# Kernel optimization log

Hardware: AMD Instinct MI355X
Metric: run time of the kernel (lower is better)

The kernel has to match this reference:

```python
import jax, jax.numpy as jnp
import numpy as np

N_NODES = 100000

def gcn_conv(x, edge_index, W, b, n_nodes):
    # GCNConv: add self-loops, symmetric normalization D^-1/2 A D^-1/2, then linear.
    loops = jnp.arange(n_nodes, dtype=edge_index.dtype)
    row = jnp.concatenate([edge_index[0], loops])  # source nodes
    col = jnp.concatenate([edge_index[1], loops])  # destination nodes
    deg = jax.ops.segment_sum(jnp.ones_like(col, dtype=x.dtype), col, num_segments=n_nodes)
    dinv = jnp.where(deg > 0, jax.lax.rsqrt(deg), 0.0)
    norm = dinv[row] * dinv[col]                   # [E']
    h = x @ W                                      # [N, out] project first (out dim small)
    msgs = h[row] * norm[:, None]                  # gather + scale
    out = jax.ops.segment_sum(msgs, col, num_segments=n_nodes)  # scatter-add
    return out + b

def setup_inputs() -> dict:
    key = jax.random.key(0)
    k1, k2, k3, k4, k5, k6 = jax.random.split(key, 6)
    in_dim, hid, out_dim = 512, 16, 16
    x = jax.random.normal(k1, (N_NODES, in_dim), dtype=jnp.float32)
    edge_index = jax.random.randint(k2, (2, 3200000), 0, N_NODES, dtype=jnp.int64)
    # Glorot-style init for weights, zero bias (GCNConv defaults)
    W1 = jax.random.normal(k3, (in_dim, hid), dtype=jnp.float32) * (1.0 / np.sqrt(in_dim))
    b1 = jnp.zeros((hid,), dtype=jnp.float32)
    W2 = jax.random.normal(k4, (hid, out_dim), dtype=jnp.float32) * (1.0 / np.sqrt(hid))
    b2 = jnp.zeros((out_dim,), dtype=jnp.float32)
    return {"x": x, "edge_index": edge_index, "W1": W1, "b1": b1, "W2": W2, "b2": b2}

def reference(x, edge_index, W1, b1, W2, b2):
    h = jax.nn.relu(gcn_conv(x, edge_index, W1, b1, N_NODES))
    # dropout is identity in eval mode
    logits = gcn_conv(h, edge_index, W2, b2, N_NODES)
    return jax.nn.log_softmax(logits, axis=1)
```

## Files before the change

### kernel.cpp

```cpp
#include <hip/hip_runtime.h>
#include <cstddef>

typedef unsigned int uint32;
typedef short bf16x8 __attribute__((ext_vector_type(8)));
typedef float f32x4 __attribute__((ext_vector_type(4)));

#define BCAP 5120

__device__ __forceinline__ unsigned short f2bf(float f) {
  unsigned u = __float_as_uint(f);
  unsigned r = (u + 0x7FFFu + ((u >> 16) & 1u)) >> 16;
  return (unsigned short)r;
}
__device__ __forceinline__ float bf_lo(uint32 u) { return __uint_as_float(u << 16); }
__device__ __forceinline__ float bf_hi(uint32 u) { return __uint_as_float(u & 0xFFFF0000u); }

__global__ __launch_bounds__(256) void k_init(
    int* __restrict__ bcur, int NB, const float* __restrict__ W1,
    unsigned short* __restrict__ wfrag) {
  int zb = (NB + 255) >> 8;
  int b = blockIdx.x;
  if (b < zb) {
    int i = b * 256 + threadIdx.x;
    if (i < NB) bcur[i] = i * BCAP;
  } else {
    int i = (b - zb) * 256 + threadIdx.x;
    if (i < 8192) {
      int j = i & 7, o = (i >> 3) & 15, g = (i >> 7) & 3, kt = i >> 9;
      wfrag[i] = f2bf(W1[(kt * 32 + g * 8 + j) * 16 + o]);
    }
  }
}

__global__ __launch_bounds__(256) void k_bfill(
    const int* __restrict__ row, const int* __restrict__ col,
    int* __restrict__ bcur, int* __restrict__ bedges, int E, int NB, int chunk) {
  __shared__ int s[1024];
  for (int j = threadIdx.x; j < NB; j += 256) s[j] = 0;
  __syncthreads();
  int lo = blockIdx.x * chunk;
  int hi = lo + chunk; if (hi > E) hi = E;
  for (int k = lo + threadIdx.x; k < hi; k += 256) atomicAdd(&s[col[k] >> 7], 1);
  __syncthreads();
  for (int j = threadIdx.x; j < NB; j += 256) {
    int h = s[j];
    s[j] = h ? atomicAdd(&bcur[j], h) : 0;
  }
  __syncthreads();
  for (int k = lo + threadIdx.x; k < hi; k += 256) {
    int c = col[k];
    int b = c >> 7;
    int slot = atomicAdd(&s[b], 1);
    if (slot < (b + 1) * BCAP)
      bedges[slot] = ((c & 127) << 17) | row[k];
  }
}

__global__ __launch_bounds__(128) void k_bdeg(
    const int* __restrict__ bcur, const int* __restrict__ bedges,
    float* __restrict__ dinv, int n) {
  __shared__ int c[128];
  int b = blockIdx.x, t = threadIdx.x;
  c[t] = 0;
  __syncthreads();
  int k0 = b * BCAP;
  int k1 = bcur[b]; if (k1 > k0 + BCAP) k1 = k0 + BCAP;
  for (int k = k0 + t; k < k1; k += 128)
    atomicAdd(&c[((unsigned)bedges[k]) >> 17], 1);
  __syncthreads();
  int node = b * 128 + t;
  if (node < n) dinv[node] = rsqrtf(1.0f + (float)c[t]);
}

#define GCAP 2048
#define CAPL 48
template <int MODE>
__global__ __launch_bounds__(256) void k_gagg(
    const int* __restrict__ bcur, const int* __restrict__ bedges,
    const uint4* __restrict__ mb,
    float* __restrict__ agg, unsigned short* __restrict__ msgs_out,
    const float* __restrict__ dinv, const float* __restrict__ b1,
    const float* __restrict__ W2, const float* __restrict__ b2, int n) {
  __shared__ int lsrt[CAPL * 128];
  __shared__ int curs[128];
  __shared__ int ovf[128];
  __shared__ int novf;
  __shared__ float w2s[256];
  __shared__ float b1s[16];
  int b = blockIdx.x, t = threadIdx.x;
  if (MODE == 1) {
    w2s[t] = W2[t];
    if (t < 16) b1s[t] = b1[t];
  }
  int j = t >> 1, h = t & 1;
  int node = b * 128 + j;
  float a0 = 0.f, a1 = 0.f, a2 = 0.f, a3 = 0.f;
  float a4 = 0.f, a5 = 0.f, a6 = 0.f, a7 = 0.f;
  if (node < n) {
    float4 sA = *(const float4*)(agg + (size_t)node * 16 + h * 8);
    float4 sB = *(const float4*)(agg + (size_t)node * 16 + h * 8 + 4);
    a0 = sA.x; a1 = sA.y; a2 = sA.z; a3 = sA.w;
    a4 = sB.x; a5 = sB.y; a6 = sB.z; a7 = sB.w;
  }
  int k0 = b * BCAP;
  int k1 = bcur[b]; if (k1 > k0 + BCAP) k1 = k0 + BCAP;
  const uint4* mbh = mb + h;
  for (int base = k0; base < k1; base += GCAP) {
    int cnt = k1 - base; if (cnt > GCAP) cnt = GCAP;
    if (t < 128) curs[t] = 0;
    if (t == 0) novf = 0;
    __syncthreads();
    for (int idx = t; idx < cnt; idx += 256) {
      unsigned e = (unsigned)bedges[base + idx];
      int lc = e >> 17;
      int slot = atomicAdd(&curs[lc], 1);
      if (slot < CAPL) lsrt[slot * 128 + lc] = (int)(e & 0x1FFFF);
      else {
        int oi = atomicAdd(&novf, 1);
        if (oi < 128) ovf[oi] = (int)e;
      }
    }
    __syncthreads();
    int len = curs[j]; if (len > CAPL) len = CAPL;
    int k = 0;
    for (; k + 4 <= len; k += 4) {
      int r0 = lsrt[(k + 0) * 128 + j], r1 = lsrt[(k + 1) * 128 + j];
      int r2 = lsrt[(k + 2) * 128 + j], r3 = lsrt[(k + 3) * 128 + j];
      uint4 v0 = mbh[(size_t)r0 * 2];
      uint4 v1 = mbh[(size_t)r1 * 2];
      uint4 v2 = mbh[(size_t)r2 * 2];
      uint4 v3 = mbh[(size_t)r3 * 2];
      a0 += (bf_lo(v0.x) + bf_lo(v1.x)) + (bf_lo(v2.x) + bf_lo(v3.x));
      a1 += (bf_hi(v0.x) + bf_hi(v1.x)) + (bf_hi(v2.x) + bf_hi(v3.x));
      a2 += (bf_lo(v0.y) + bf_lo(v1.y)) + (bf_lo(v2.y) + bf_lo(v3.y));
      a3 += (bf_hi(v0.y) + bf_hi(v1.y)) + (bf_hi(v2.y) + bf_hi(v3.y));
      a4 += (bf_lo(v0.z) + bf_lo(v1.z)) + (bf_lo(v2.z) + bf_lo(v3.z));
      a5 += (bf_hi(v0.z) + bf_hi(v1.z)) + (bf_hi(v2.z) + bf_hi(v3.z));
      a6 += (bf_lo(v0.w) + bf_lo(v1.w)) + (bf_lo(v2.w) + bf_lo(v3.w));
      a7 += (bf_hi(v0.w) + bf_hi(v1.w)) + (bf_hi(v2.w) + bf_hi(v3.w));
    }
    for (; k < len; ++k) {
      uint4 v = mbh[(size_t)lsrt[k * 128 + j] * 2];
      a0 += bf_lo(v.x); a1 += bf_hi(v.x);
      a2 += bf_lo(v.y); a3 += bf_hi(v.y);
      a4 += bf_lo(v.z); a5 += bf_hi(v.z);
      a6 += bf_lo(v.w); a7 += bf_hi(v.w);
    }
    int no = novf; if (no > 128) no = 128;
    for (int i = 0; i < no; ++i) {
      unsigned e = (unsigned)ovf[i];
      if ((int)(e >> 17) == j) {
        uint4 v = mbh[(size_t)(e & 0x1FFFF) * 2];
        a0 += bf_lo(v.x); a1 += bf_hi(v.x);
        a2 += bf_lo(v.y); a3 += bf_hi(v.y);
        a4 += bf_lo(v.z); a5 += bf_hi(v.z);
        a6 += bf_lo(v.w); a7 += bf_hi(v.w);
      }
    }
    __syncthreads();
  }
  if (node < n) {
    float tot[8] = {a0, a1, a2, a3, a4, a5, a6, a7};
    float di = dinv[node];
    if (MODE == 1) {
      float hh[8];
#pragma unroll
      for (int f = 0; f < 8; ++f)
        hh[f] = fmaxf(fmaf(di, tot[f], b1s[h * 8 + f]), 0.0f);
      float gp[16];
#pragma unroll
      for (int o = 0; o < 16; ++o) gp[o] = 0.0f;
#pragma unroll
      for (int f = 0; f < 8; ++f) {
        float hf = hh[f];
        const float* wrow = &w2s[(h * 8 + f) * 16];
#pragma unroll
        for (int o = 0; o < 16; ++o) gp[o] = fmaf(hf, wrow[o], gp[o]);
      }
      float gv[8];
#pragma unroll
      for (int f = 0; f < 8; ++f) {
        float keep = h ? gp[8 + f] : gp[f];
        float send = h ? gp[f] : gp[8 + f];
        gv[f] = (keep + __shfl_xor(send, 1, 64)) * di;
      }
      uint32 u0 = (uint32)f2bf(gv[0]) | ((uint32)f2bf(gv[1]) << 16);
      uint32 u1 = (uint32)f2bf(gv[2]) | ((uint32)f2bf(gv[3]) << 16);
      uint32 u2 = (uint32)f2bf(gv[4]) | ((uint32)f2bf(gv[5]) << 16);
      uint32 u3 = (uint32)f2bf(gv[6]) | ((uint32)f2bf(gv[7]) << 16);
      uint4 pk; pk.x = u0; pk.y = u1; pk.z = u2; pk.w = u3;
      ((uint4*)msgs_out)[(size_t)node * 2 + h] = pk;
      float4* aw = (float4*)(agg + (size_t)node * 16 + h * 8);
      aw[0] = make_float4(gv[0], gv[1], gv[2], gv[3]);
      aw[1] = make_float4(gv[4], gv[5], gv[6], gv[7]);
    } else {
      float v[8];
#pragma unroll
      for (int f = 0; f < 8; ++f) v[f] = fmaf(di, tot[f], b2[h * 8 + f]);
      float m8 = v[0];
#pragma unroll
      for (int f = 1; f < 8; ++f) m8 = fmaxf(m8, v[f]);
      float m = fmaxf(m8, __shfl_xor(m8, 1, 64));
      float s8 = 0.0f;
#pragma unroll
      for (int f = 0; f < 8; ++f) s8 += expf(v[f] - m);
      float s = s8 + __shfl_xor(s8, 1, 64);
      float ls = logf(s) + m;
      float4* aw = (float4*)(agg + (size_t)node * 16 + h * 8);
      aw[0] = make_float4(v[0] - ls, v[1] - ls, v[2] - ls, v[3] - ls);
      aw[1] = make_float4(v[4] - ls, v[5] - ls, v[6] - ls, v[7] - ls);
    }
  }
}

__global__ __launch_bounds__(256) void k_gemm1_mfma(
    const float* __restrict__ x, const uint4* __restrict__ wf4,
    const float* __restrict__ dinv, unsigned short* __restrict__ msgsb,
    float* __restrict__ agg, int n) {
  int wave = threadIdx.x >> 6, lane = threadIdx.x & 63;
  int m = lane & 15, g = lane >> 4;
  int r0 = (blockIdx.x * 4 + wave) * 16;
  if (r0 >= n) return;

  union BU { uint4 u; bf16x8 v; };
  BU bfr[16];
#pragma unroll
  for (int kt = 0; kt < 16; ++kt) bfr[kt].u = wf4[kt * 64 + g * 16 + m];

  int row = r0 + m;
  int lrow = (row < n) ? row : (n - 1);
  const float* xr = x + (size_t)lrow * 512 + g * 8;

  f32x4 acc = {0.f, 0.f, 0.f, 0.f};
#pragma unroll
  for (int kt = 0; kt < 16; ++kt) {
    float4 xa = *(const float4*)(xr + kt * 32);
    float4 xb = *(const float4*)(xr + kt * 32 + 4);
    union { uint32 u[4]; bf16x8 v; } a;
    a.u[0] = (uint32)f2bf(xa.x) | ((uint32)f2bf(xa.y) << 16);
    a.u[1] = (uint32)f2bf(xa.z) | ((uint32)f2bf(xa.w) << 16);
    a.u[2] = (uint32)f2bf(xb.x) | ((uint32)f2bf(xb.y) << 16);
    a.u[3] = (uint32)f2bf(xb.z) | ((uint32)f2bf(xb.w) << 16);
    acc = __builtin_amdgcn_mfma_f32_16x16x32_bf16(a.v, bfr[kt].v, acc, 0, 0, 0);
  }

#pragma unroll
  for (int j = 0; j < 4; ++j) {
    int orow = r0 + g * 4 + j;
    if (orow < n) {
      float v = acc[j] * dinv[orow];
      agg[(size_t)orow * 16 + m] = v;
      msgsb[(size_t)orow * 16 + m] = f2bf(v);
    }
  }
}


__global__ void k_deg_init(float* __restrict__ deg, int n) {
  int i = blockIdx.x * 256 + threadIdx.x;
  if (i < n) deg[i] = 1.0f;
}

__global__ void k_deg_count(const int* __restrict__ col, float* __restrict__ deg, int E) {
  int e = blockIdx.x * 256 + threadIdx.x;
  if (e < E) atomicAdd(&deg[col[e]], 1.0f);
}

__global__ void k_rsqrt_inplace(float* __restrict__ deg, int n) {
  int i = blockIdx.x * 256 + threadIdx.x;
  if (i < n) deg[i] = rsqrtf(deg[i]);
}

__global__ void k_scatter(const int* __restrict__ row, const int* __restrict__ col,
                          const float* __restrict__ src, float* __restrict__ agg, int E) {
  int t = blockIdx.x * 256 + threadIdx.x;
  int e = t >> 2, q = t & 3;
  if (e >= E) return;
  int r = row[e];
  int c = col[e];
  float4 v = ((const float4*)(src + (size_t)r * 16))[q];
  float* dst = agg + (size_t)c * 16 + q * 4;
  atomicAdd(dst + 0, v.x);
  atomicAdd(dst + 1, v.y);
  atomicAdd(dst + 2, v.z);
  atomicAdd(dst + 3, v.w);
}

__global__ void k_transposeW1(const float* __restrict__ W1, float* __restrict__ wt) {
  int i = blockIdx.x * 256 + threadIdx.x;
  if (i < 512 * 16) {
    int e = i >> 4, f = i & 15;
    wt[f * 512 + e] = W1[i];
  }
}

__global__ __launch_bounds__(256) void k_gemm1(
    const float* __restrict__ x, const float* __restrict__ wt_g,
    const float* __restrict__ dinv,
    float* __restrict__ msgsf, float* __restrict__ agg, int n) {
  __shared__ float4 wt4[16 * 128];
  const float4* wg4 = (const float4*)wt_g;
  for (int k = threadIdx.x; k < 2048; k += 256) wt4[k] = wg4[k];
  __syncthreads();

  int wave = threadIdx.x >> 6, lane = threadIdx.x & 63;
  int r0 = blockIdx.x * 8 + wave * 2;
  if (r0 >= n) return;
  int r1 = (r0 + 1 < n) ? (r0 + 1) : r0;

  const float4* x0 = (const float4*)(x + (size_t)r0 * 512);
  const float4* x1 = (const float4*)(x + (size_t)r1 * 512);
  float4 xa0 = x0[lane], xb0 = x0[64 + lane];
  float4 xa1 = x1[lane], xb1 = x1[64 + lane];

  float acc0[16], acc1[16];
#pragma unroll
  for (int f = 0; f < 16; ++f) {
    float4 wa = wt4[f * 128 + lane];
    float4 wb = wt4[f * 128 + 64 + lane];
    acc0[f] = xa0.x * wa.x + xa0.y * wa.y + xa0.z * wa.z + xa0.w * wa.w +
              xb0.x * wb.x + xb0.y * wb.y + xb0.z * wb.z + xb0.w * wb.w;
    acc1[f] = xa1.x * wa.x + xa1.y * wa.y + xa1.z * wa.z + xa1.w * wa.w +
              xb1.x * wb.x + xb1.y * wb.y + xb1.z * wb.z + xb1.w * wb.w;
  }

#pragma unroll
  for (int s = 0; s < 4; ++s) {
    const int mask = 1 << s;
    const int hm = 8 >> s;
    bool up = (lane & mask) != 0;
#pragma unroll
    for (int i = 0; i < hm; ++i) {
      float s0 = up ? acc0[i] : acc0[i + hm];
      float s1 = up ? acc1[i] : acc1[i + hm];
      float g0 = __shfl_xor(s0, mask, 64);
      float g1 = __shfl_xor(s1, mask, 64);
      acc0[i] = (up ? acc0[i + hm] : acc0[i]) + g0;
      acc1[i] = (up ? acc1[i + hm] : acc1[i]) + g1;
    }
  }
  acc0[0] += __shfl_xor(acc0[0], 16, 64);
  acc0[0] += __shfl_xor(acc0[0], 32, 64);
  acc1[0] += __shfl_xor(acc1[0], 16, 64);
  acc1[0] += __shfl_xor(acc1[0], 32, 64);

  int grp = lane >> 4;
  if (grp < 2) {
    int row = r0 + grp;
    if (row < n) {
      int l4 = lane & 15;
      int f = ((l4 & 1) << 3) | ((l4 & 2) << 1) | ((l4 & 4) >> 1) | ((l4 & 8) >> 3);
      float v = (grp == 0 ? acc0[0] : acc1[0]) * dinv[row];
      msgsf[(size_t)row * 16 + f] = v;
      agg[(size_t)row * 16 + f] = v;
    }
  }
}

__global__ __launch_bounds__(256) void k_mid(
    float* __restrict__ agg, const float* __restrict__ dinv,
    const float* __restrict__ b1, const float* __restrict__ W2,
    float* __restrict__ gpf, int n) {
  __shared__ float w2s[256];
  __shared__ float b1s[16];
  if (threadIdx.x < 256) w2s[threadIdx.x] = W2[threadIdx.x];
  if (threadIdx.x < 16) b1s[threadIdx.x] = b1[threadIdx.x];
  __syncthreads();
  int i = blockIdx.x * 256 + threadIdx.x;
  if (i >= n) return;
  float di = dinv[i];
  float h[16];
  const float4* a4 = (const float4*)(agg + (size_t)i * 16);
#pragma unroll
  for (int q = 0; q < 4; ++q) {
    float4 v = a4[q];
    h[q * 4 + 0] = v.x; h[q * 4 + 1] = v.y; h[q * 4 + 2] = v.z; h[q * 4 + 3] = v.w;
  }
#pragma unroll
  for (int f = 0; f < 16; ++f) h[f] = fmaxf(fmaf(di, h[f], b1s[f]), 0.0f);
  float g[16];
#pragma unroll
  for (int o = 0; o < 16; ++o) g[o] = 0.0f;
#pragma unroll
  for (int f = 0; f < 16; ++f) {
    float hf = h[f];
#pragma unroll
    for (int o = 0; o < 16; ++o) g[o] = fmaf(hf, w2s[f * 16 + o], g[o]);
  }
  float4* gA = (float4*)(gpf + (size_t)i * 16);
  float4* gB = (float4*)(agg + (size_t)i * 16);
#pragma unroll
  for (int q = 0; q < 4; ++q) {
    float4 v;
    v.x = g[q * 4 + 0] * di; v.y = g[q * 4 + 1] * di;
    v.z = g[q * 4 + 2] * di; v.w = g[q * 4 + 3] * di;
    gA[q] = v;
    gB[q] = v;
  }
}

__global__ __launch_bounds__(256) void k_final(
    float* __restrict__ agg, const float* __restrict__ dinv,
    const float* __restrict__ b2, int n) {
  int i = blockIdx.x * 256 + threadIdx.x;
  if (i >= n) return;
  float di = dinv[i];
  float v[16];
  const float4* a4 = (const float4*)(agg + (size_t)i * 16);
#pragma unroll
  for (int q = 0; q < 4; ++q) {
    float4 t = a4[q];
    v[q * 4 + 0] = t.x; v[q * 4 + 1] = t.y; v[q * 4 + 2] = t.z; v[q * 4 + 3] = t.w;
  }
#pragma unroll
  for (int f = 0; f < 16; ++f) v[f] = fmaf(di, v[f], b2[f]);
  float m = v[0];
#pragma unroll
  for (int f = 1; f < 16; ++f) m = fmaxf(m, v[f]);
  float s = 0.0f;
#pragma unroll
  for (int f = 0; f < 16; ++f) s += expf(v[f] - m);
  float ls = logf(s) + m;
  float4* o4 = (float4*)(agg + (size_t)i * 16);
#pragma unroll
  for (int q = 0; q < 4; ++q) {
    float4 t;
    t.x = v[q * 4 + 0] - ls; t.y = v[q * 4 + 1] - ls;
    t.z = v[q * 4 + 2] - ls; t.w = v[q * 4 + 3] - ls;
    o4[q] = t;
  }
}

extern "C" void kernel_launch(void* const* d_in, const int* in_sizes, int n_in,
                              void* d_out, int out_size, void* d_ws, size_t ws_size,
                              hipStream_t stream) {
  const float* x = (const float*)d_in[0];
  const int* ei = (const int*)d_in[1];
  const float* W1 = (const float*)d_in[2];
  const float* b1 = (const float*)d_in[3];
  const float* W2 = (const float*)d_in[4];
  const float* b2 = (const float*)d_in[5];
  float* out = (float*)d_out;

  int n = in_sizes[0] / 512;
  int E = in_sizes[1] / 2;
  const int* row = ei;
  const int* col = ei + E;
  int NB = (n + 127) >> 7;

  auto align1k = [](size_t v) { return (v + 1023) & ~(size_t)1023; };
  char* ws = (char*)d_ws;
  size_t o = 0;
  float* dinv  = (float*)(ws + o); o += align1k((size_t)n * 4);
  unsigned short* wfrag = (unsigned short*)(ws + o); o += align1k(8192 * 2);
  int* bcur    = (int*)(ws + o);   o += align1k((size_t)NB * 4);
  int* bedges  = (int*)(ws + o);   o += align1k((size_t)NB * BCAP * 4);
  unsigned short* msgsb1 = (unsigned short*)(ws + o); o += align1k((size_t)n * 16 * 2);
  unsigned short* msgsb2 = (unsigned short*)(ws + o); o += align1k((size_t)n * 16 * 2);
  size_t needed = o;

  float* agg = out;
  int nb_n = (n + 255) / 256;
  int nb_e = (E + 255) / 256;
  int nb_e4 = (E * 4 + 255) / 256;

  if (ws_size >= needed && n <= 131072 && NB <= 1024) {
    const int NBLK = 256;
    int chunk = (E + NBLK - 1) / NBLK;
    int zb = (NB + 255) >> 8;
    k_init<<<zb + 32, 256, 0, stream>>>(bcur, NB, W1, wfrag);
    k_bfill<<<NBLK, 256, 0, stream>>>(row, col, bcur, bedges, E, NB, chunk);
    k_bdeg<<<NB, 128, 0, stream>>>(bcur, bedges, dinv, n);
    k_gemm1_mfma<<<(n + 63) / 64, 256, 0, stream>>>(
        x, (const uint4*)wfrag, dinv, msgsb1, agg, n);
    k_gagg<1><<<NB, 256, 0, stream>>>(
        bcur, bedges, (const uint4*)msgsb1, agg, msgsb2, dinv, b1, W2, b2, n);
    k_gagg<2><<<NB, 256, 0, stream>>>(
        bcur, bedges, (const uint4*)msgsb2, agg, nullptr, dinv, b1, W2, b2, n);
  } else {
    size_t o2 = 0;
    float* dinv2 = (float*)(ws + o2); o2 += align1k((size_t)n * 4);
    float* wtg2  = (float*)(ws + o2); o2 += 32768;
    float* msgs2 = (float*)(ws + o2);
    k_deg_init<<<nb_n, 256, 0, stream>>>(dinv2, n);
    k_deg_count<<<nb_e, 256, 0, stream>>>(col, dinv2, E);
    k_rsqrt_inplace<<<nb_n, 256, 0, stream>>>(dinv2, n);
    k_transposeW1<<<32, 256, 0, stream>>>(W1, wtg2);
    k_gemm1<<<(n + 7) / 8, 256, 0, stream>>>(x, wtg2, dinv2, msgs2, agg, n);
    k_scatter<<<nb_e4, 256, 0, stream>>>(row, col, msgs2, agg, E);
    k_mid<<<nb_n, 256, 0, stream>>>(agg, dinv2, b1, W2, msgs2, n);
    k_scatter<<<nb_e4, 256, 0, stream>>>(row, col, msgs2, agg, E);
    k_final<<<nb_n, 256, 0, stream>>>(agg, dinv2, b2, n);
  }
}
```

Before: 191.1 us.

## Fuse edge bucketing with layer-1 GEMM and defer dinv scaling to aggregation

Merges the edge bucket-fill kernel and the MFMA projection GEMM into one launch, so the memory-bound edge binning and the x@W1 GEMM can run concurrently on different blocks. The W1 bf16 fragment is now built per block in shared memory instead of by a separate init kernel. Because the GEMM no longer waits on degrees, the source-side dinv scaling moves into layer-1 aggregation as a per-edge dinv gather, and the self-loop term is scaled by the destination dinv. This adds an extra random 4-byte load per edge in the first aggregation and drops bf16 rounding of the scaled values, in exchange for removing a serial kernel dependency and the init kernel.

```diff
diff --git a/kernel.cpp b/kernel.cpp
--- a/kernel.cpp
+++ b/kernel.cpp
@@ -6,6 +6,7 @@
 typedef float f32x4 __attribute__((ext_vector_type(4)));
 
 #define BCAP 5120
+#define NBLK 256
 
 __device__ __forceinline__ unsigned short f2bf(float f) {
   unsigned u = __float_as_uint(f);
@@ -15,44 +16,81 @@
 __device__ __forceinline__ float bf_lo(uint32 u) { return __uint_as_float(u << 16); }
 __device__ __forceinline__ float bf_hi(uint32 u) { return __uint_as_float(u & 0xFFFF0000u); }
 
-__global__ __launch_bounds__(256) void k_init(
-    int* __restrict__ bcur, int NB, const float* __restrict__ W1,
-    unsigned short* __restrict__ wfrag) {
-  int zb = (NB + 255) >> 8;
-  int b = blockIdx.x;
-  if (b < zb) {
-    int i = b * 256 + threadIdx.x;
-    if (i < NB) bcur[i] = i * BCAP;
-  } else {
-    int i = (b - zb) * 256 + threadIdx.x;
-    if (i < 8192) {
-      int j = i & 7, o = (i >> 3) & 15, g = (i >> 7) & 3, kt = i >> 9;
-      wfrag[i] = f2bf(W1[(kt * 32 + g * 8 + j) * 16 + o]);
-    }
-  }
-}
-
-__global__ __launch_bounds__(256) void k_bfill(
+__global__ void k_zero_i(int* __restrict__ p, int n) {
+  int i = blockIdx.x * 256 + threadIdx.x;
+  if (i < n) p[i] = 0;
+}
+
+__global__ __launch_bounds__(256) void k_fused(
     const int* __restrict__ row, const int* __restrict__ col,
-    int* __restrict__ bcur, int* __restrict__ bedges, int E, int NB, int chunk) {
-  __shared__ int s[1024];
-  for (int j = threadIdx.x; j < NB; j += 256) s[j] = 0;
+    int* __restrict__ bcur, int* __restrict__ bedges,
+    const float* __restrict__ W1, const float* __restrict__ x,
+    unsigned short* __restrict__ msgsb, float* __restrict__ agg,
+    int E, int NB, int chunk, int n) {
+  __shared__ unsigned short wl[8192];
+  int blk = blockIdx.x;
+  if (blk < NBLK) {
+    int* s = (int*)wl;
+    for (int j = threadIdx.x; j < NB; j += 256) s[j] = 0;
+    __syncthreads();
+    int lo = blk * chunk;
+    int hi = lo + chunk; if (hi > E) hi = E;
+    for (int k = lo + threadIdx.x; k < hi; k += 256) atomicAdd(&s[col[k] >> 7], 1);
+    __syncthreads();
+    for (int j = threadIdx.x; j < NB; j += 256) {
+      int h = s[j];
+      s[j] = h ? atomicAdd(&bcur[j], h) : 0;
+    }
+    __syncthreads();
+    for (int k = lo + threadIdx.x; k < hi; k += 256) {
+      int c = col[k];
+      int b = c >> 7;
+      int off = atomicAdd(&s[b], 1);
+      if (off < BCAP)
+        bedges[(size_t)b * BCAP + off] = ((c & 127) << 17) | row[k];
+    }
+    return;
+  }
+  for (int i = threadIdx.x; i < 8192; i += 256) {
+    int j = i & 7, o = (i >> 3) & 15, g = (i >> 7) & 3, kt = i >> 9;
+    wl[i] = f2bf(W1[(kt * 32 + g * 8 + j) * 16 + o]);
+  }
   __syncthreads();
-  int lo = blockIdx.x * chunk;
-  int hi = lo + chunk; if (hi > E) hi = E;
-  for (int k = lo + threadIdx.x; k < hi; k += 256) atomicAdd(&s[col[k] >> 7], 1);
-  __syncthreads();
-  for (int j = threadIdx.x; j < NB; j += 256) {
-    int h = s[j];
-    s[j] = h ? atomicAdd(&bcur[j], h) : 0;
-  }
-  __syncthreads();
-  for (int k = lo + threadIdx.x; k < hi; k += 256) {
-    int c = col[k];
-    int b = c >> 7;
-    int slot = atomicAdd(&s[b], 1);
-    if (slot < (b + 1) * BCAP)
-      bedges[slot] = ((c & 127) << 17) | row[k];
+  int gb = blk - NBLK;
+  int wave = threadIdx.x >> 6, lane = threadIdx.x & 63;
+  int m = lane & 15, g = lane >> 4;
+  int r0 = (gb * 4 + wave) * 16;
+  if (r0 >= n) return;
+
+  const uint4* wf4 = (const uint4*)wl;
+  union BU { uint4 u; bf16x8 v; };
+  BU bfr[16];
+#pragma unroll
+  for (int kt = 0; kt < 16; ++kt) bfr[kt].u = wf4[kt * 64 + g * 16 + m];
+
+  int rw = r0 + m;
+  int lrow = (rw < n) ? rw : (n - 1);
+  const float* xr = x + (size_t)lrow * 512 + g * 8;
+
+  f32x4 acc = {0.f, 0.f, 0.f, 0.f};
+#pragma unroll
+  for (int kt = 0; kt < 16; ++kt) {
+    float4 xa = *(const float4*)(xr + kt * 32);
+    float4 xb = *(const float4*)(xr + kt * 32 + 4);
+    union { uint32 u[4]; bf16x8 v; } a;
+    a.u[0] = (uint32)f2bf(xa.x) | ((uint32)f2bf(xa.y) << 16);
+    a.u[1] = (uint32)f2bf(xa.z) | ((uint32)f2bf(xa.w) << 16);
+    a.u[2] = (uint32)f2bf(xb.x) | ((uint32)f2bf(xb.y) << 16);
+    a.u[3] = (uint32)f2bf(xb.z) | ((uint32)f2bf(xb.w) << 16);
+    acc = __builtin_amdgcn_mfma_f32_16x16x32_bf16(a.v, bfr[kt].v, acc, 0, 0, 0);
+  }
+#pragma unroll
+  for (int j = 0; j < 4; ++j) {
+    int orow = r0 + g * 4 + j;
+    if (orow < n) {
+      agg[(size_t)orow * 16 + m] = acc[j];
+      msgsb[(size_t)orow * 16 + m] = f2bf(acc[j]);
+    }
   }
 }
 
@@ -64,8 +102,8 @@
   c[t] = 0;
   __syncthreads();
   int k0 = b * BCAP;
-  int k1 = bcur[b]; if (k1 > k0 + BCAP) k1 = k0 + BCAP;
-  for (int k = k0 + t; k < k1; k += 128)
+  int cnt = bcur[b]; if (cnt > BCAP) cnt = BCAP;
+  for (int k = k0 + t; k < k0 + cnt; k += 128)
     atomicAdd(&c[((unsigned)bedges[k]) >> 17], 1);
   __syncthreads();
   int node = b * 128 + t;
@@ -94,23 +132,26 @@
   }
   int j = t >> 1, h = t & 1;
   int node = b * 128 + j;
+  float di = (node < n) ? dinv[node] : 0.0f;
   float a0 = 0.f, a1 = 0.f, a2 = 0.f, a3 = 0.f;
   float a4 = 0.f, a5 = 0.f, a6 = 0.f, a7 = 0.f;
   if (node < n) {
     float4 sA = *(const float4*)(agg + (size_t)node * 16 + h * 8);
     float4 sB = *(const float4*)(agg + (size_t)node * 16 + h * 8 + 4);
-    a0 = sA.x; a1 = sA.y; a2 = sA.z; a3 = sA.w;
-    a4 = sB.x; a5 = sB.y; a6 = sB.z; a7 = sB.w;
+    float ss = (MODE == 1) ? di : 1.0f;
+    a0 = ss * sA.x; a1 = ss * sA.y; a2 = ss * sA.z; a3 = ss * sA.w;
+    a4 = ss * sB.x; a5 = ss * sB.y; a6 = ss * sB.z; a7 = ss * sB.w;
   }
   int k0 = b * BCAP;
-  int k1 = bcur[b]; if (k1 > k0 + BCAP) k1 = k0 + BCAP;
+  int cnt = bcur[b]; if (cnt > BCAP) cnt = BCAP;
+  int k1 = k0 + cnt;
   const uint4* mbh = mb + h;
   for (int base = k0; base < k1; base += GCAP) {
-    int cnt = k1 - base; if (cnt > GCAP) cnt = GCAP;
+    int tc = k1 - base; if (tc > GCAP) tc = GCAP;
     if (t < 128) curs[t] = 0;
     if (t == 0) novf = 0;
     __syncthreads();
-    for (int idx = t; idx < cnt; idx += 256) {
+    for (int idx = t; idx < tc; idx += 256) {
       unsigned e = (unsigned)bedges[base + idx];
       int lc = e >> 17;
       int slot = atomicAdd(&curs[lc], 1);
@@ -130,38 +171,43 @@
       uint4 v1 = mbh[(size_t)r1 * 2];
       uint4 v2 = mbh[(size_t)r2 * 2];
       uint4 v3 = mbh[(size_t)r3 * 2];
-      a0 += (bf_lo(v0.x) + bf_lo(v1.x)) + (bf_lo(v2.x) + bf_lo(v3.x));
-      a1 += (bf_hi(v0.x) + bf_hi(v1.x)) + (bf_hi(v2.x) + bf_hi(v3.x));
-      a2 += (bf_lo(v0.y) + bf_lo(v1.y)) + (bf_lo(v2.y) + bf_lo(v3.y));
-      a3 += (bf_hi(v0.y) + bf_hi(v1.y)) + (bf_hi(v2.y) + bf_hi(v3.y));
-      a4 += (bf_lo(v0.z) + bf_lo(v1.z)) + (bf_lo(v2.z) + bf_lo(v3.z));
-      a5 += (bf_hi(v0.z) + bf_hi(v1.z)) + (bf_hi(v2.z) + bf_hi(v3.z));
-      a6 += (bf_lo(v0.w) + bf_lo(v1.w)) + (bf_lo(v2.w) + bf_lo(v3.w));
-      a7 += (bf_hi(v0.w) + bf_hi(v1.w)) + (bf_hi(v2.w) + bf_hi(v3.w));
+      float d0 = 1.f, d1 = 1.f, d2 = 1.f, d3 = 1.f;
+      if (MODE == 1) { d0 = dinv[r0]; d1 = dinv[r1]; d2 = dinv[r2]; d3 = dinv[r3]; }
+      a0 += (d0 * bf_lo(v0.x) + d1 * bf_lo(v1.x)) + (d2 * bf_lo(v2.x) + d3 * bf_lo(v3.x));
+      a1 += (d0 * bf_hi(v0.x) + d1 * bf_hi(v1.x)) + (d2 * bf_hi(v2.x) + d3 * bf_hi(v3.x));
+      a2 += (d0 * bf_lo(v0.y) + d1 * bf_lo(v1.y)) + (d2 * bf_lo(v2.y) + d3 * bf_lo(v3.y));
+      a3 += (d0 * bf_hi(v0.y) + d1 * bf_hi(v1.y)) + (d2 * bf_hi(v2.y) + d3 * bf_hi(v3.y));
+      a4 += (d0 * bf_lo(v0.z) + d1 * bf_lo(v1.z)) + (d2 * bf_lo(v2.z) + d3 * bf_lo(v3.z));
+      a5 += (d0 * bf_hi(v0.z) + d1 * bf_hi(v1.z)) + (d2 * bf_hi(v2.z) + d3 * bf_hi(v3.z));
+      a6 += (d0 * bf_lo(v0.w) + d1 * bf_lo(v1.w)) + (d2 * bf_lo(v2.w) + d3 * bf_lo(v3.w));
+      a7 += (d0 * bf_hi(v0.w) + d1 * bf_hi(v1.w)) + (d2 * bf_hi(v2.w) + d3 * bf_hi(v3.w));
     }
     for (; k < len; ++k) {
-      uint4 v = mbh[(size_t)lsrt[k * 128 + j] * 2];
-      a0 += bf_lo(v.x); a1 += bf_hi(v.x);
-      a2 += bf_lo(v.y); a3 += bf_hi(v.y);
-      a4 += bf_lo(v.z); a5 += bf_hi(v.z);
-      a6 += bf_lo(v.w); a7 += bf_hi(v.w);
+      int r = lsrt[k * 128 + j];
+      uint4 v = mbh[(size_t)r * 2];
+      float d = (MODE == 1) ? dinv[r] : 1.0f;
+      a0 += d * bf_lo(v.x); a1 += d * bf_hi(v.x);
+      a2 += d * bf_lo(v.y); a3 += d * bf_hi(v.y);
+      a4 += d * bf_lo(v.z); a5 += d * bf_hi(v.z);
+      a6 += d * bf_lo(v.w); a7 += d * bf_hi(v.w);
     }
     int no = novf; if (no > 128) no = 128;
     for (int i = 0; i < no; ++i) {
       unsigned e = (unsigned)ovf[i];
       if ((int)(e >> 17) == j) {
-        uint4 v = mbh[(size_t)(e & 0x1FFFF) * 2];
-        a0 += bf_lo(v.x); a1 += bf_hi(v.x);
-        a2 += bf_lo(v.y); a3 += bf_hi(v.y);
-        a4 += bf_lo(v.z); a5 += bf_hi(v.z);
-        a6 += bf_lo(v.w); a7 += bf_hi(v.w);
+        int r = (int)(e & 0x1FFFF);
+        uint4 v = mbh[(size_t)r * 2];
+        float d = (MODE == 1) ? dinv[r] : 1.0f;
+        a0 += d * bf_lo(v.x); a1 += d * bf_hi(v.x);
+        a2 += d * bf_lo(v.y); a3 += d * bf_hi(v.y);
+        a4 += d * bf_lo(v.z); a5 += d * bf_hi(v.z);
+        a6 += d * bf_lo(v.w); a7 += d * bf_hi(v.w);
       }
     }
     __syncthreads();
   }
   if (node < n) {
     float tot[8] = {a0, a1, a2, a3, a4, a5, a6, a7};
-    float di = dinv[node];
     if (MODE == 1) {
       float hh[8];
 #pragma unroll
@@ -213,48 +259,6 @@
   }
 }
 
-__global__ __launch_bounds__(256) void k_gemm1_mfma(
-    const float* __restrict__ x, const uint4* __restrict__ wf4,
-    const float* __restrict__ dinv, unsigned short* __restrict__ msgsb,
-    float* __restrict__ agg, int n) {
-  int wave = threadIdx.x >> 6, lane = threadIdx.x & 63;
-  int m = lane & 15, g = lane >> 4;
-  int r0 = (blockIdx.x * 4 + wave) * 16;
-  if (r0 >= n) return;
-
-  union BU { uint4 u; bf16x8 v; };
-  BU bfr[16];
-#pragma unroll
-  for (int kt = 0; kt < 16; ++kt) bfr[kt].u = wf4[kt * 64 + g * 16 + m];
-
-  int row = r0 + m;
-  int lrow = (row < n) ? row : (n - 1);
-  const float* xr = x + (size_t)lrow * 512 + g * 8;
-
-  f32x4 acc = {0.f, 0.f, 0.f, 0.f};
-#pragma unroll
-  for (int kt = 0; kt < 16; ++kt) {
-    float4 xa = *(const float4*)(xr + kt * 32);
-    float4 xb = *(const float4*)(xr + kt * 32 + 4);
-    union { uint32 u[4]; bf16x8 v; } a;
-    a.u[0] = (uint32)f2bf(xa.x) | ((uint32)f2bf(xa.y) << 16);
-    a.u[1] = (uint32)f2bf(xa.z) | ((uint32)f2bf(xa.w) << 16);
-    a.u[2] = (uint32)f2bf(xb.x) | ((uint32)f2bf(xb.y) << 16);
-    a.u[3] = (uint32)f2bf(xb.z) | ((uint32)f2bf(xb.w) << 16);
-    acc = __builtin_amdgcn_mfma_f32_16x16x32_bf16(a.v, bfr[kt].v, acc, 0, 0, 0);
-  }
-
-#pragma unroll
-  for (int j = 0; j < 4; ++j) {
-    int orow = r0 + g * 4 + j;
-    if (orow < n) {
-      float v = acc[j] * dinv[orow];
-      agg[(size_t)orow * 16 + m] = v;
-      msgsb[(size_t)orow * 16 + m] = f2bf(v);
-    }
-  }
-}
-
 
 __global__ void k_deg_init(float* __restrict__ deg, int n) {
   int i = blockIdx.x * 256 + threadIdx.x;
@@ -452,7 +456,6 @@
   char* ws = (char*)d_ws;
   size_t o = 0;
   float* dinv  = (float*)(ws + o); o += align1k((size_t)n * 4);
-  unsigned short* wfrag = (unsigned short*)(ws + o); o += align1k(8192 * 2);
   int* bcur    = (int*)(ws + o);   o += align1k((size_t)NB * 4);
   int* bedges  = (int*)(ws + o);   o += align1k((size_t)NB * BCAP * 4);
   unsigned short* msgsb1 = (unsigned short*)(ws + o); o += align1k((size_t)n * 16 * 2);
@@ -465,14 +468,12 @@
   int nb_e4 = (E * 4 + 255) / 256;
 
   if (ws_size >= needed && n <= 131072 && NB <= 1024) {
-    const int NBLK = 256;
     int chunk = (E + NBLK - 1) / NBLK;
-    int zb = (NB + 255) >> 8;
-    k_init<<<zb + 32, 256, 0, stream>>>(bcur, NB, W1, wfrag);
-    k_bfill<<<NBLK, 256, 0, stream>>>(row, col, bcur, bedges, E, NB, chunk);
+    int gemm_blocks = (n + 63) / 64;
+    k_zero_i<<<(NB + 255) / 256, 256, 0, stream>>>(bcur, NB);
+    k_fused<<<NBLK + gemm_blocks, 256, 0, stream>>>(
+        row, col, bcur, bedges, W1, x, msgsb1, agg, E, NB, chunk, n);
     k_bdeg<<<NB, 128, 0, stream>>>(bcur, bedges, dinv, n);
-    k_gemm1_mfma<<<(n + 63) / 64, 256, 0, stream>>>(
-        x, (const uint4*)wfrag, dinv, msgsb1, agg, n);
     k_gagg<1><<<NB, 256, 0, stream>>>(
         bcur, bedges, (const uint4*)msgsb1, agg, msgsb2, dinv, b1, W2, b2, n);
     k_gagg<2><<<NB, 256, 0, stream>>>(
```

Result: slower. 196.0 us (+2.6%).
